# Kernel tuning notes

Measured on AMD Instinct MI355X. Metric: run time of the kernel, lower is better.

## Reference

```python
import jax, jax.numpy as jnp
import numpy as np

IMG, P, C = 512, 16, 1
D, DEPTH, H, DH, MLP = 768, 12, 8, 64, 2048
GRID = IMG // P          # 32
NP = GRID * GRID         # 1024 patches
N = NP + 1               # +cls token
EPS = 1e-5


def _ln(x, s, b):
    m = jnp.mean(x, -1, keepdims=True)
    v = jnp.mean((x - m) ** 2, -1, keepdims=True)
    return (x - m) * jax.lax.rsqrt(v + EPS) * s + b


def setup_inputs() -> dict:
    key = jax.random.key(0)
    ks = jax.random.split(key, 12)
    s = 0.02
    f32 = jnp.float32
    return {
        "x": jax.random.normal(ks[0], (4, C, IMG, IMG), f32),
        "conv_w": jax.random.normal(ks[1], (D, C, P, P), f32) * s,   # [out,in,kh,kw] like torch
        "conv_b": jnp.zeros((D,), f32),
        "cls_token": jax.random.normal(ks[2], (1, 1, D), f32),
        "pos_emb": jax.random.normal(ks[3], (1, N, D), f32),
        "qkv_w": jax.random.normal(ks[4], (DEPTH, D, 3 * H * DH), f32) * s,  # [in,out] layout
        "merge_w": jax.random.normal(ks[5], (DEPTH, H * DH, D), f32) * s,
        "merge_b": jnp.zeros((DEPTH, D), f32),
        "ln1_s": jnp.ones((DEPTH, D), f32),
        "ln1_b": jnp.zeros((DEPTH, D), f32),
        "ln2_s": jnp.ones((DEPTH, D), f32),
        "ln2_b": jnp.zeros((DEPTH, D), f32),
        "ffn_w1": jax.random.normal(ks[6], (DEPTH, D, MLP), f32) * s,
        "ffn_b1": jnp.zeros((DEPTH, MLP), f32),
        "ffn_w2": jax.random.normal(ks[7], (DEPTH, MLP, D), f32) * s,
        "ffn_b2": jnp.zeros((DEPTH, D), f32),
        "lnf_s": jnp.ones((D,), f32),
        "lnf_b": jnp.zeros((D,), f32),
    }


def reference(x, conv_w, conv_b, cls_token, pos_emb, qkv_w, merge_w, merge_b,
              ln1_s, ln1_b, ln2_s, ln2_b, ffn_w1, ffn_b1, ffn_w2, ffn_b2,
              lnf_s, lnf_b):
    B = x.shape[0]
    # Patch embed: stride-P conv == non-overlapping patch extraction + matmul
    xr = x.reshape(B, C, GRID, P, GRID, P)
    tok = jnp.einsum('bchpwq,dcpq->bhwd', xr, conv_w).reshape(B, NP, D) + conv_b
    t = jnp.concatenate([jnp.broadcast_to(cls_token, (B, 1, D)), tok], axis=1)
    t = t + pos_emb  # dropout is identity in eval
    scale = DH ** -0.5
    for i in range(DEPTH):
        # MSA with pre-LN
        h = _ln(t, ln1_s[i], ln1_b[i])
        qkv = (h @ qkv_w[i]).reshape(B, N, H, 3, DH)   # [B,N,H,3,DH]
        q = jnp.transpose(qkv[..., 0, :], (0, 2, 1, 3))  # [B,H,N,DH]
        k = jnp.transpose(qkv[..., 1, :], (0, 2, 1, 3))
        v = jnp.transpose(qkv[..., 2, :], (0, 2, 1, 3))
        att = jax.nn.softmax(jnp.einsum('bhnd,bhmd->bhnm', q, k) * scale, axis=-1)
        o = jnp.einsum('bhnm,bhmd->bhnd', att, v)
        o = jnp.transpose(o, (0, 2, 1, 3)).reshape(B, N, H * DH)
        t = t + (o @ merge_w[i] + merge_b[i])
        # FFN with pre-LN, exact (erf) GELU like torch nn.GELU
        h2 = _ln(t, ln2_s[i], ln2_b[i])
        f = jax.nn.gelu(h2 @ ffn_w1[i] + ffn_b1[i], approximate=False)
        t = t + (f @ ffn_w2[i] + ffn_b2[i])
    return _ln(t, lnf_s, lnf_b)
```

## Files before the change

### kernel.cpp

```cpp
#include <hip/hip_runtime.h>

#define DEV __device__ __forceinline__

typedef short s4v __attribute__((ext_vector_type(4)));
typedef short s8v __attribute__((ext_vector_type(8)));
typedef float f4v __attribute__((ext_vector_type(4)));
typedef unsigned int u32x2 __attribute__((ext_vector_type(2)));

DEV short f2bf(float f) {
  unsigned u = __float_as_uint(f);
  u += 0x7FFFu + ((u >> 16) & 1u);
  return (short)(u >> 16);
}
DEV short f2bf_fast(float f) {
  return (short)((__float_as_uint(f) + 0x8000u) >> 16);
}
DEV float bf2f(short s) { return __uint_as_float(((unsigned)(unsigned short)s) << 16); }

DEV void gld_lds16(const short* g, short* l) {
  __builtin_amdgcn_global_load_lds(
      (const __attribute__((address_space(1))) void*)g,
      (__attribute__((address_space(3))) void*)l, 16, 0, 0);
}

DEV u32x2 trr(unsigned lds_byte) {
  u32x2 r;
  asm volatile("ds_read_b64_tr_b16 %0, %1" : "=&v"(r) : "v"(lds_byte));
  return r;
}

DEV int xcd_swz(int id, int nwg) {
  int q8 = nwg >> 3, r8 = nwg & 7, xcd = id & 7, off = id >> 3;
  return (xcd < r8) ? (xcd * (q8 + 1) + off) : (r8 * (q8 + 1) + (xcd - r8) * q8 + off);
}

template<int BN>
__global__ __launch_bounds__(256) void gemm_t(
    const short* __restrict__ A, const short* __restrict__ B, void* __restrict__ Cv,
    const float* __restrict__ bias,
    int M, int N, int K, int lda, int ldb, int ldc, int flags)
{
  constexpr int BPASS = BN / 32;
  constexpr int MI = (BN == 128) ? 4 : 2;
  __shared__ __align__(16) short As[2][64 * 64];
  __shared__ __align__(16) short Bs[2][BN * 64];
  int nwg = gridDim.x * gridDim.y;
  int idl = blockIdx.y * gridDim.x + blockIdx.x;
  int swz = xcd_swz(idl, nwg);
  int bx = swz % gridDim.x, by = swz / gridDim.x;
  int m0 = by * 64, n0 = bx * BN;
  int tid = threadIdx.x, lane = tid & 63, w = tid >> 6;
  int lr = lane & 15, kg = lane >> 4;
  int wrb = (BN == 128) ? 0 : (w >> 1) * 32;
  int wcb = (BN == 128) ? w * 32 : (w & 1) * 32;
  f4v acc[MI][2] = {};
  int NT = K >> 6;

#define STAGE(bufi, k0)                                                   \
  {                                                                       \
    _Pragma("unroll")                                                     \
    for (int p = 0; p < 2; ++p) {                                         \
      int ch = p * 256 + w * 64 + lane;                                   \
      int row = ch >> 3, c = (ch & 7) ^ (row & 7);                        \
      gld_lds16(A + (long)(m0 + row) * lda + (k0) + c * 8,                \
                &As[bufi][(p * 256 + w * 64) * 8]);                       \
    }                                                                     \
    _Pragma("unroll")                                                     \
    for (int p = 0; p < BPASS; ++p) {                                     \
      int ch = p * 256 + w * 64 + lane;                                   \
      int row = ch >> 3, c = (ch & 7) ^ (row & 7);                        \
      gld_lds16(B + (long)(n0 + row) * ldb + (k0) + c * 8,                \
                &Bs[bufi][(p * 256 + w * 64) * 8]);                       \
    }                                                                     \
  }

  STAGE(0, 0)
  for (int t = 0; t < NT; ++t) {
    int buf = t & 1;
    if (t + 1 < NT) {
      STAGE(buf ^ 1, (t + 1) * 64)
      if constexpr (BN == 128)
        asm volatile("s_waitcnt vmcnt(6)" ::: "memory");
      else
        asm volatile("s_waitcnt vmcnt(4)" ::: "memory");
    } else {
      asm volatile("s_waitcnt vmcnt(0)" ::: "memory");
    }
    __builtin_amdgcn_s_barrier();
    #pragma unroll
    for (int ks = 0; ks < 2; ++ks) {
      s8v av[MI], bv[2];
      #pragma unroll
      for (int mi = 0; mi < MI; ++mi) {
        int row = wrb + mi * 16 + lr;
        int sl = (ks * 4 + kg) ^ (row & 7);
        av[mi] = *(const s8v*)&As[buf][row * 64 + sl * 8];
      }
      #pragma unroll
      for (int ni = 0; ni < 2; ++ni) {
        int row = wcb + ni * 16 + lr;
        int sl = (ks * 4 + kg) ^ (row & 7);
        bv[ni] = *(const s8v*)&Bs[buf][row * 64 + sl * 8];
      }
      #pragma unroll
      for (int mi = 0; mi < MI; ++mi)
        #pragma unroll
        for (int ni = 0; ni < 2; ++ni)
          acc[mi][ni] = __builtin_amdgcn_mfma_f32_16x16x32_bf16(av[mi], bv[ni], acc[mi][ni], 0, 0, 0);
    }
    asm volatile("s_waitcnt lgkmcnt(0)" ::: "memory");
    __builtin_amdgcn_s_barrier();
  }
#undef STAGE

  float* Cf = (float*)Cv;
  short* Cb = (short*)Cv;
  #pragma unroll
  for (int mi = 0; mi < MI; ++mi)
    #pragma unroll
    for (int ni = 0; ni < 2; ++ni) {
      int col = n0 + wcb + ni * 16 + lr;
      float bvv = (flags & 1) ? bias[col] : 0.f;
      #pragma unroll
      for (int j = 0; j < 4; ++j) {
        int row = m0 + wrb + mi * 16 + kg * 4 + j;
        if (row >= M) continue;
        float v = acc[mi][ni][j] + bvv;
        if (flags & 2) v = 0.5f * v * (1.f + erff(v * 0.70710678118f));
        long ci = (long)row * ldc + col;
        if (flags & 8) Cb[ci] = f2bf(v);
        else { if (flags & 4) v += Cf[ci]; Cf[ci] = v; }
      }
    }
}

__global__ __launch_bounds__(512) void flash_k(
    const short* __restrict__ qkv, short* __restrict__ O)
{
  int swz = xcd_swz(blockIdx.x, 544);
  int z = swz / 17, qt = swz - z * 17;
  int zb = z >> 3, zh = z & 7;
  const short* base = qkv + (long)zb * 1025 * 1536 + zh * 192;
  const short* Qg = base;
  const short* Kg = base + 64;
  const short* Vg = base + 128;
  int q0 = qt * 64;
  int tid = threadIdx.x, lane = tid & 63, w = tid >> 6;
  int g = w >> 2, wl = w & 3;
  int lr = lane & 15, kg = lane >> 4;
  int kt0 = g * 8;

  __shared__ __align__(16) short Ks[2][2][64 * 64];
  __shared__ __align__(16) short Vs[2][2][64 * 64];

  s8v aq[2];
  {
    long qrow = q0 + wl * 16 + lr;
    aq[0] = *(const s8v*)(Qg + qrow * 1536 + kg * 8);
    aq[1] = *(const s8v*)(Qg + qrow * 1536 + 32 + kg * 8);
  }

  unsigned vsbase = (unsigned)(unsigned long long)
      (__attribute__((address_space(3))) void*)&Vs[0][0][0];
  unsigned vtr = (unsigned)(lr * 8 + kg * 1024);

#define STAGE_K(bufi, kv0)                                                 \
  {                                                                        \
    int s0 = wl * 128;                                                     \
    _Pragma("unroll")                                                      \
    for (int i = 0; i < 2; ++i) {                                          \
      int s = s0 + i * 64 + lane;                                          \
      int row = s >> 3, c = (s & 7) ^ (row & 7);                           \
      gld_lds16(Kg + (long)((kv0) + row) * 1536 + c * 8,                   \
                &Ks[g][bufi][(s0 + i * 64) * 8]);                          \
    }                                                                      \
  }
#define STAGE_V(bufi, kv0)                                                 \
  {                                                                        \
    int s0 = wl * 128;                                                     \
    _Pragma("unroll")                                                      \
    for (int i = 0; i < 2; ++i) {                                          \
      int ch = s0 + i * 64 + lane;                                         \
      int st = ch >> 3, r = (ch & 7) >> 1, hh = ch & 1;                    \
      int key = (kv0) + (st >> 2) * 4 + r;                                 \
      int d = (st & 3) * 16 + hh * 8;                                      \
      gld_lds16(Vg + (long)key * 1536 + d,                                 \
                &Vs[g][bufi][(s0 + i * 64) * 8]);                          \
    }                                                                      \
  }

  f4v acc[4] = {};
  float m_run = -3.0e38f, l_run = 0.f;
  const float C2 = 0.18033688011112042f;
  const float THR = 44.36f;

  STAGE_K(0, kt0 * 64)
  STAGE_V(0, kt0 * 64)
  asm volatile("s_waitcnt vmcnt(0)" ::: "memory");
  __builtin_amdgcn_s_barrier();

  for (int kt = kt0; kt < kt0 + 8; ++kt) {
    int cur = (kt - kt0) & 1;
    if (kt + 1 < kt0 + 8) {
      STAGE_K(cur ^ 1, (kt + 1) * 64)
      STAGE_V(cur ^ 1, (kt + 1) * 64)
    }

    f4v sa[4] = {};
    __builtin_amdgcn_s_setprio(1);
    #pragma unroll
    for (int ni = 0; ni < 4; ++ni) {
      int row = ni * 16 + lr;
      #pragma unroll
      for (int ks = 0; ks < 2; ++ks) {
        int c = (ks * 4 + kg) ^ (row & 7);
        s8v kf = *(const s8v*)&Ks[g][cur][row * 64 + c * 8];
        sa[ni] = __builtin_amdgcn_mfma_f32_16x16x32_bf16(kf, aq[ks], sa[ni], 0, 0, 0);
      }
    }
    __builtin_amdgcn_s_setprio(0);

    float tm = -3.0e38f;
    #pragma unroll
    for (int ni = 0; ni < 4; ++ni)
      #pragma unroll
      for (int jj = 0; jj < 4; ++jj) tm = fmaxf(tm, sa[ni][jj]);
    tm = fmaxf(tm, __shfl_xor(tm, 16));
    tm = fmaxf(tm, __shfl_xor(tm, 32));
    bool need = !__all(tm <= m_run + THR);
    float scale = 1.f;
    if (need) {
      float m_new = fmaxf(m_run, tm);
      scale = exp2f((m_run - m_new) * C2);
      m_run = m_new;
    }
    float mC = m_run * C2;
    float pv[4][4];
    float ts = 0.f;
    #pragma unroll
    for (int ni = 0; ni < 4; ++ni)
      #pragma unroll
      for (int jj = 0; jj < 4; ++jj) {
        float p = exp2f(fmaf(sa[ni][jj], C2, -mC));
        pv[ni][jj] = p;
        ts += p;
      }
    ts += __shfl_xor(ts, 16);
    ts += __shfl_xor(ts, 32);
    l_run = l_run * scale + ts;
    if (need) {
      float scq[4];
      #pragma unroll
      for (int jj = 0; jj < 4; ++jj)
        scq[jj] = __shfl(scale, kg * 4 + jj + 16 * kg);
      #pragma unroll
      for (int ni = 0; ni < 4; ++ni)
        #pragma unroll
        for (int jj = 0; jj < 4; ++jj) acc[ni][jj] *= scq[jj];
    }

    unsigned pr[4][2];
    #pragma unroll
    for (int ni = 0; ni < 4; ++ni)
      #pragma unroll
      for (int hh = 0; hh < 2; ++hh) {
        unsigned lo = (unsigned)(unsigned short)f2bf_fast(pv[ni][2 * hh]);
        unsigned hi = (unsigned)(unsigned short)f2bf_fast(pv[ni][2 * hh + 1]);
        pr[ni][hh] = lo | (hi << 16);
      }
    union PU { s8v v; unsigned u[4]; };
    PU apu[2];
    #pragma unroll
    for (int ks = 0; ks < 2; ++ks)
      #pragma unroll
      for (int t = 0; t < 4; ++t) {
        unsigned src = (kg & 2) ? pr[2 * ks + 1][t & 1] : pr[2 * ks][t & 1];
        apu[ks].u[t] = __shfl(src, lr + 16 * (2 * (kg & 1) + (t >> 1)));
      }

    u32x2 tr[4][2][2];
    unsigned vb = vsbase + (unsigned)(g * 2 + cur) * 8192u + vtr;
    #pragma unroll
    for (int ni = 0; ni < 4; ++ni)
      #pragma unroll
      for (int ks = 0; ks < 2; ++ks) {
        tr[ni][ks][0] = trr(vb + ni * 128 + ks * 4096);
        tr[ni][ks][1] = trr(vb + ni * 128 + ks * 4096 + 512);
      }
    asm volatile("s_waitcnt lgkmcnt(0)" ::: "memory");
    __builtin_amdgcn_sched_barrier(0);

    __builtin_amdgcn_s_setprio(1);
    #pragma unroll
    for (int ni = 0; ni < 4; ++ni) {
      #pragma unroll
      for (int ks = 0; ks < 2; ++ks) {
        union { s8v v; u32x2 u2[2]; } bb;
        bb.u2[0] = tr[ni][ks][0];
        bb.u2[1] = tr[ni][ks][1];
        acc[ni] = __builtin_amdgcn_mfma_f32_16x16x32_bf16(apu[ks].v, bb.v, acc[ni], 0, 0, 0);
      }
    }
    __builtin_amdgcn_s_setprio(0);
    asm volatile("s_waitcnt lgkmcnt(0)" ::: "memory");
    asm volatile("s_waitcnt vmcnt(0)" ::: "memory");
    __builtin_amdgcn_s_barrier();
  }
#undef STAGE_K
#undef STAGE_V

  if (g) {
    s8v k0 = *(const s8v*)(Kg + 1024L * 1536 + kg * 8);
    s8v k1 = *(const s8v*)(Kg + 1024L * 1536 + 32 + kg * 8);
    float s = 0.f;
    #pragma unroll
    for (int j = 0; j < 8; ++j)
      s += bf2f(aq[0][j]) * bf2f(k0[j]) + bf2f(aq[1][j]) * bf2f(k1[j]);
    s += __shfl_xor(s, 16);
    s += __shfl_xor(s, 32);
    float m_new = fmaxf(m_run, s);
    float sc = exp2f((m_run - m_new) * C2);
    float p = exp2f((s - m_new) * C2);
    m_run = m_new;
    l_run = l_run * sc + p;
    float vrow[4];
    #pragma unroll
    for (int ni = 0; ni < 4; ++ni)
      vrow[ni] = bf2f(Vg[1024L * 1536 + ni * 16 + lr]);
    float scq[4], pq[4];
    #pragma unroll
    for (int jj = 0; jj < 4; ++jj) {
      scq[jj] = __shfl(sc, kg * 4 + jj + 16 * kg);
      pq[jj]  = __shfl(p,  kg * 4 + jj + 16 * kg);
    }
    #pragma unroll
    for (int ni = 0; ni < 4; ++ni)
      #pragma unroll
      for (int jj = 0; jj < 4; ++jj)
        acc[ni][jj] = acc[ni][jj] * scq[jj] + pq[jj] * vrow[ni];
  }

  float* AccL = (float*)&Ks[0][0][0];
  float* MLs  = (float*)&Vs[0][0][0];
  if (kg == 0) {
    MLs[(g * 64 + wl * 16 + lr) * 2]     = m_run;
    MLs[(g * 64 + wl * 16 + lr) * 2 + 1] = l_run;
  }
  if (g == 0) {
    #pragma unroll
    for (int ni = 0; ni < 4; ++ni)
      #pragma unroll
      for (int jj = 0; jj < 4; ++jj)
        AccL[(wl * 16 + kg * 4 + jj) * 64 + ni * 16 + lr] = acc[ni][jj];
  }
  asm volatile("s_waitcnt lgkmcnt(0)" ::: "memory");
  __builtin_amdgcn_s_barrier();
  if (g == 1) {
    float m0 = MLs[(wl * 16 + lr) * 2], l0 = MLs[(wl * 16 + lr) * 2 + 1];
    float M = fmaxf(m0, m_run);
    float w0 = exp2f((m0 - M) * C2), w1 = exp2f((m_run - M) * C2);
    float inv = 1.f / (l0 * w0 + l_run * w1);
    float c0 = w0 * inv, c1 = w1 * inv;
    float c0q[4], c1q[4];
    #pragma unroll
    for (int jj = 0; jj < 4; ++jj) {
      c0q[jj] = __shfl(c0, kg * 4 + jj + 16 * kg);
      c1q[jj] = __shfl(c1, kg * 4 + jj + 16 * kg);
    }
    #pragma unroll
    for (int ni = 0; ni < 4; ++ni)
      #pragma unroll
      for (int jj = 0; jj < 4; ++jj) {
        int row = q0 + wl * 16 + kg * 4 + jj;
        if (row < 1025) {
          float a0 = AccL[(wl * 16 + kg * 4 + jj) * 64 + ni * 16 + lr];
          O[((long)(zb * 1025 + row)) * 512 + zh * 64 + ni * 16 + lr] =
              f2bf(a0 * c0q[jj] + acc[ni][jj] * c1q[jj]);
        }
      }
  }
}

DEV void tconv_body(const float* w, short* wt, int K, int N, int bx, int by, int tid)
{
  __shared__ float tile[32][33];
  int n0 = bx * 32, k0 = by * 32;
  int tx = tid & 31, ty = tid >> 5;
  #pragma unroll
  for (int j = 0; j < 4; ++j)
    tile[ty + j * 8][tx] = w[(long)(k0 + ty + j * 8) * N + n0 + tx];
  __syncthreads();
  #pragma unroll
  for (int j = 0; j < 4; ++j)
    wt[(long)(n0 + ty + j * 8) * K + k0 + tx] = f2bf(tile[tx][ty + j * 8]);
}

__global__ __launch_bounds__(256) void tconv4_k(
    const float* __restrict__ sq, const float* __restrict__ sm,
    const float* __restrict__ sf1, const float* __restrict__ sf2,
    short* __restrict__ dq, short* __restrict__ dm,
    short* __restrict__ df1, short* __restrict__ df2)
{
  int id = blockIdx.x, tid = threadIdx.x;
  if (id < 1152)       tconv_body(sq,  dq,  768, 1536, id % 48,          id / 48,          tid);
  else if (id < 1536)  tconv_body(sm,  dm,  512, 768,  (id - 1152) % 24, (id - 1152) / 24, tid);
  else if (id < 3072)  tconv_body(sf1, df1, 768, 2048, (id - 1536) % 64, (id - 1536) / 64, tid);
  else                 tconv_body(sf2, df2, 2048, 768, (id - 3072) % 24, (id - 3072) / 24, tid);
}

__global__ __launch_bounds__(256) void cvt_k(const float* __restrict__ in,
    short* __restrict__ out, int n)
{
  int i = blockIdx.x * 256 + threadIdx.x;
  if (i < n) out[i] = f2bf(in[i]);
}

DEV void st4(float* p, f4v v) { *(f4v*)p = v; }
DEV void st4(short* p, f4v v) {
  s4v o = { f2bf(v[0]), f2bf(v[1]), f2bf(v[2]), f2bf(v[3]) };
  *(s4v*)p = o;
}

template<typename OT>
__global__ __launch_bounds__(256) void ln_k(const float* __restrict__ x,
    const float* __restrict__ g, const float* __restrict__ b,
    OT* __restrict__ y, int rows)
{
  int row = blockIdx.x * 4 + (threadIdx.x >> 6);
  if (row >= rows) return;
  int lane = threadIdx.x & 63;
  const float* xr = x + (long)row * 768;
  f4v v[3];
  #pragma unroll
  for (int i = 0; i < 3; ++i) v[i] = *(const f4v*)(xr + i * 256 + lane * 4);
  float s = 0.f, s2 = 0.f;
  #pragma unroll
  for (int i = 0; i < 3; ++i)
    #pragma unroll
    for (int j = 0; j < 4; ++j) { s += v[i][j]; s2 += v[i][j] * v[i][j]; }
  #pragma unroll
  for (int o = 1; o < 64; o <<= 1) { s += __shfl_xor(s, o); s2 += __shfl_xor(s2, o); }
  float mean = s * (1.f / 768.f);
  float var = s2 * (1.f / 768.f) - mean * mean;
  float r = rsqrtf(var + 1e-5f);
  OT* yr = y + (long)row * 768;
  #pragma unroll
  for (int i = 0; i < 3; ++i) {
    f4v gg = *(const f4v*)(g + i * 256 + lane * 4);
    f4v bb = *(const f4v*)(b + i * 256 + lane * 4);
    f4v o;
    #pragma unroll
    for (int j = 0; j < 4; ++j) o[j] = (v[i][j] - mean) * r * gg[j] + bb[j];
    st4(yr + i * 256 + lane * 4, o);
  }
}

__global__ __launch_bounds__(256) void im2col_k(const float* __restrict__ x,
    short* __restrict__ A)
{
  int i = blockIdx.x * 256 + threadIdx.x;
  int k = i & 255, row = i >> 8;
  int px = k & 15, py = k >> 4;
  int gx = row & 31, gy = (row >> 5) & 31, b = row >> 10;
  A[i] = f2bf(x[((long)(b * 512) + gy * 16 + py) * 512 + gx * 16 + px]);
}

__global__ __launch_bounds__(256) void assemble_k(const short* __restrict__ tok,
    const float* __restrict__ cls, const float* __restrict__ pos, float* __restrict__ t)
{
  int i = blockIdx.x * 256 + threadIdx.x;
  int d = i % 768; int rn = i / 768; int n = rn % 1025; int b = rn / 1025;
  float v = (n == 0) ? cls[d] : bf2f(tok[((long)(b * 1024 + n - 1)) * 768 + d]);
  t[i] = v + pos[n * 768 + d];
}

extern "C" void kernel_launch(void* const* d_in, const int* in_sizes, int n_in,
                              void* d_out, int out_size, void* d_ws, size_t ws_size,
                              hipStream_t stream)
{
  const float* x       = (const float*)d_in[0];
  const float* conv_w  = (const float*)d_in[1];
  const float* conv_b  = (const float*)d_in[2];
  const float* cls     = (const float*)d_in[3];
  const float* pos     = (const float*)d_in[4];
  const float* qkv_w   = (const float*)d_in[5];
  const float* merge_w = (const float*)d_in[6];
  const float* merge_b = (const float*)d_in[7];
  const float* ln1_s   = (const float*)d_in[8];
  const float* ln1_b   = (const float*)d_in[9];
  const float* ln2_s   = (const float*)d_in[10];
  const float* ln2_b   = (const float*)d_in[11];
  const float* ffn_w1  = (const float*)d_in[12];
  const float* ffn_b1  = (const float*)d_in[13];
  const float* ffn_w2  = (const float*)d_in[14];
  const float* ffn_b2  = (const float*)d_in[15];
  const float* lnf_s   = (const float*)d_in[16];
  const float* lnf_b   = (const float*)d_in[17];

  char* wsp = (char*)d_ws;
  size_t o = 0;
  auto take = [&](size_t bytes) { char* r = wsp + o; o = (o + bytes + 255) & ~(size_t)255; return r; };
  short* wq   = (short*)take(1536ul * 768 * 2);
  short* wm   = (short*)take(768ul * 512 * 2);
  short* wf1  = (short*)take(2048ul * 768 * 2);
  short* wf2  = (short*)take(768ul * 2048 * 2);
  short* wcv  = (short*)take(768ul * 256 * 2);
  float* t    = (float*)take(4100ul * 768 * 4);
  char*  hO   = take(4352ul * 768 * 2);
  short* qkv  = (short*)take(4ul * 1025 * 1536 * 2);
  char*  fV   = take(4352ul * 2048 * 2);
  take(2ul << 20);

  short* h   = (short*)hO;
  short* O   = (short*)hO;
  short* f   = (short*)fV;
  short* imc = (short*)fV;
  short* tok = (short*)(fV + 4096ul * 256 * 2);

  dim3 blk(256), blk512(512);

  cvt_k<<<768, blk, 0, stream>>>(conv_w, wcv, 768 * 256);
  im2col_k<<<4096, blk, 0, stream>>>(x, imc);
  gemm_t<64><<<dim3(12, 64), blk, 0, stream>>>(imc, wcv, tok, conv_b,
      4096, 768, 256, 256, 256, 768, 1 | 8);
  assemble_k<<<12300, blk, 0, stream>>>(tok, cls, pos, t);

  for (int i = 0; i < 12; ++i) {
    tconv4_k<<<4608, blk, 0, stream>>>(
        qkv_w + (long)i * 768 * 1536, merge_w + (long)i * 512 * 768,
        ffn_w1 + (long)i * 768 * 2048, ffn_w2 + (long)i * 2048 * 768,
        wq, wm, wf1, wf2);

    ln_k<short><<<1025, blk, 0, stream>>>(t, ln1_s + i * 768, ln1_b + i * 768, h, 4100);
    gemm_t<64><<<dim3(24, 65), blk, 0, stream>>>(h, wq, qkv, nullptr,
        4100, 1536, 768, 768, 768, 1536, 8);
    flash_k<<<544, blk512, 0, stream>>>(qkv, O);
    gemm_t<64><<<dim3(12, 65), blk, 0, stream>>>(O, wm, t, merge_b + i * 768,
        4100, 768, 512, 512, 512, 768, 1 | 4);
    ln_k<short><<<1025, blk, 0, stream>>>(t, ln2_s + i * 768, ln2_b + i * 768, h, 4100);
    gemm_t<64><<<dim3(32, 65), blk, 0, stream>>>(h, wf1, f, ffn_b1 + i * 2048,
        4100, 2048, 768, 768, 768, 2048, 1 | 2 | 8);
    gemm_t<64><<<dim3(12, 65), blk, 0, stream>>>(f, wf2, t, ffn_b2 + i * 768,
        4100, 768, 2048, 2048, 2048, 768, 1 | 4);
  }
  ln_k<float><<<1025, blk, 0, stream>>>(t, lnf_s, lnf_b, (float*)d_out, 4100);
}
```

Before: 1.969 ms.

## Split-K the N=768 projection GEMMs and fold partial-sum reduction into LayerNorm

The merge and FFN2 GEMMs, which have only 12x65 tiles, now run with a 2-way K split into two fp32 partial buffers, giving twice as many workgroups to fill the GPU. The following LayerNorm kernel adds both partials into the residual, writes the updated residual back, and normalizes it. This replaces the read-modify-write residual epilogue. The cost is extra fp32 partial-buffer traffic, about 25MB of writes and reads per GEMM, and an extra residual store in the LN kernel.

```diff
diff --git a/kernel.cpp b/kernel.cpp
--- a/kernel.cpp
+++ b/kernel.cpp
@@ -38,7 +38,7 @@
 __global__ __launch_bounds__(256) void gemm_t(
     const short* __restrict__ A, const short* __restrict__ B, void* __restrict__ Cv,
     const float* __restrict__ bias,
-    int M, int N, int K, int lda, int ldb, int ldc, int flags)
+    int M, int N, int K, int lda, int ldb, int ldc, int flags, int ksplit, long zCoff)
 {
   constexpr int BPASS = BN / 32;
   constexpr int MI = (BN == 128) ? 4 : 2;
@@ -54,7 +54,9 @@
   int wrb = (BN == 128) ? 0 : (w >> 1) * 32;
   int wcb = (BN == 128) ? w * 32 : (w & 1) * 32;
   f4v acc[MI][2] = {};
-  int NT = K >> 6;
+  int KH = K / ksplit;
+  int kbase = blockIdx.z * KH;
+  int NT = KH >> 6;
 
 #define STAGE(bufi, k0)                                                   \
   {                                                                       \
@@ -74,11 +76,11 @@
     }                                                                     \
   }
 
-  STAGE(0, 0)
+  STAGE(0, kbase)
   for (int t = 0; t < NT; ++t) {
     int buf = t & 1;
     if (t + 1 < NT) {
-      STAGE(buf ^ 1, (t + 1) * 64)
+      STAGE(buf ^ 1, kbase + (t + 1) * 64)
       if constexpr (BN == 128)
         asm volatile("s_waitcnt vmcnt(6)" ::: "memory");
       else
@@ -113,14 +115,15 @@
   }
 #undef STAGE
 
-  float* Cf = (float*)Cv;
-  short* Cb = (short*)Cv;
+  float* Cf = (float*)Cv + blockIdx.z * zCoff;
+  short* Cb = (short*)Cv + blockIdx.z * zCoff;
+  bool dob = (flags & 1) && blockIdx.z == 0;
   #pragma unroll
   for (int mi = 0; mi < MI; ++mi)
     #pragma unroll
     for (int ni = 0; ni < 2; ++ni) {
       int col = n0 + wcb + ni * 16 + lr;
-      float bvv = (flags & 1) ? bias[col] : 0.f;
+      float bvv = dob ? bias[col] : 0.f;
       #pragma unroll
       for (int j = 0; j < 4; ++j) {
         int row = m0 + wrb + mi * 16 + kg * 4 + j;
@@ -423,16 +426,30 @@
 
 template<typename OT>
 __global__ __launch_bounds__(256) void ln_k(const float* __restrict__ x,
+    const float* __restrict__ P0, const float* __restrict__ P1,
     const float* __restrict__ g, const float* __restrict__ b,
-    OT* __restrict__ y, int rows)
+    OT* __restrict__ y, float* __restrict__ xout, int rows)
 {
   int row = blockIdx.x * 4 + (threadIdx.x >> 6);
   if (row >= rows) return;
   int lane = threadIdx.x & 63;
-  const float* xr = x + (long)row * 768;
+  long rb = (long)row * 768;
   f4v v[3];
   #pragma unroll
-  for (int i = 0; i < 3; ++i) v[i] = *(const f4v*)(xr + i * 256 + lane * 4);
+  for (int i = 0; i < 3; ++i) v[i] = *(const f4v*)(x + rb + i * 256 + lane * 4);
+  if (P0) {
+    #pragma unroll
+    for (int i = 0; i < 3; ++i) {
+      f4v p0 = *(const f4v*)(P0 + rb + i * 256 + lane * 4);
+      f4v p1 = *(const f4v*)(P1 + rb + i * 256 + lane * 4);
+      #pragma unroll
+      for (int j = 0; j < 4; ++j) v[i][j] += p0[j] + p1[j];
+    }
+    if (xout) {
+      #pragma unroll
+      for (int i = 0; i < 3; ++i) st4(xout + rb + i * 256 + lane * 4, v[i]);
+    }
+  }
   float s = 0.f, s2 = 0.f;
   #pragma unroll
   for (int i = 0; i < 3; ++i)
@@ -443,7 +460,7 @@
   float mean = s * (1.f / 768.f);
   float var = s2 * (1.f / 768.f) - mean * mean;
   float r = rsqrtf(var + 1e-5f);
-  OT* yr = y + (long)row * 768;
+  OT* yr = y + rb;
   #pragma unroll
   for (int i = 0; i < 3; ++i) {
     f4v gg = *(const f4v*)(g + i * 256 + lane * 4);
@@ -506,6 +523,7 @@
   short* wf2  = (short*)take(768ul * 2048 * 2);
   short* wcv  = (short*)take(768ul * 256 * 2);
   float* t    = (float*)take(4100ul * 768 * 4);
+  float* PA   = (float*)take(2ul * 4100 * 768 * 4);
   char*  hO   = take(4352ul * 768 * 2);
   short* qkv  = (short*)take(4ul * 1025 * 1536 * 2);
   char*  fV   = take(4352ul * 2048 * 2);
@@ -516,13 +534,14 @@
   short* f   = (short*)fV;
   short* imc = (short*)fV;
   short* tok = (short*)(fV + 4096ul * 256 * 2);
+  const long PZ = 4100L * 768;
 
   dim3 blk(256), blk512(512);
 
   cvt_k<<<768, blk, 0, stream>>>(conv_w, wcv, 768 * 256);
   im2col_k<<<4096, blk, 0, stream>>>(x, imc);
   gemm_t<64><<<dim3(12, 64), blk, 0, stream>>>(imc, wcv, tok, conv_b,
-      4096, 768, 256, 256, 256, 768, 1 | 8);
+      4096, 768, 256, 256, 256, 768, 1 | 8, 1, 0);
   assemble_k<<<12300, blk, 0, stream>>>(tok, cls, pos, t);
 
   for (int i = 0; i < 12; ++i) {
@@ -531,17 +550,20 @@
         ffn_w1 + (long)i * 768 * 2048, ffn_w2 + (long)i * 2048 * 768,
         wq, wm, wf1, wf2);
 
-    ln_k<short><<<1025, blk, 0, stream>>>(t, ln1_s + i * 768, ln1_b + i * 768, h, 4100);
+    ln_k<short><<<1025, blk, 0, stream>>>(t, i ? PA : nullptr, PA + PZ,
+        ln1_s + i * 768, ln1_b + i * 768, h, t, 4100);
     gemm_t<64><<<dim3(24, 65), blk, 0, stream>>>(h, wq, qkv, nullptr,
-        4100, 1536, 768, 768, 768, 1536, 8);
+        4100, 1536, 768, 768, 768, 1536, 8, 1, 0);
     flash_k<<<544, blk512, 0, stream>>>(qkv, O);
-    gemm_t<64><<<dim3(12, 65), blk, 0, stream>>>(O, wm, t, merge_b + i * 768,
-        4100, 768, 512, 512, 512, 768, 1 | 4);
-    ln_k<short><<<1025, blk, 0, stream>>>(t, ln2_s + i * 768, ln2_b + i * 768, h, 4100);
+    gemm_t<64><<<dim3(12, 65, 2), blk, 0, stream>>>(O, wm, PA, merge_b + i * 768,
+        4100, 768, 512, 512, 512, 768, 1, 2, PZ);
+    ln_k<short><<<1025, blk, 0, stream>>>(t, PA, PA + PZ,
+        ln2_s + i * 768, ln2_b + i * 768, h, t, 4100);
     gemm_t<64><<<dim3(32, 65), blk, 0, stream>>>(h, wf1, f, ffn_b1 + i * 2048,
-        4100, 2048, 768, 768, 768, 2048, 1 | 2 | 8);
-    gemm_t<64><<<dim3(12, 65), blk, 0, stream>>>(f, wf2, t, ffn_b2 + i * 768,
-        4100, 768, 2048, 2048, 2048, 768, 1 | 4);
-  }
-  ln_k<float><<<1025, blk, 0, stream>>>(t, lnf_s, lnf_b, (float*)d_out, 4100);
-}
+        4100, 2048, 768, 768, 768, 2048, 1 | 2 | 8, 1, 0);
+    gemm_t<64><<<dim3(12, 65, 2), blk, 0, stream>>>(f, wf2, PA, ffn_b2 + i * 768,
+        4100, 768, 2048, 2048, 2048, 768, 1, 2, PZ);
+  }
+  ln_k<float><<<1025, blk, 0, stream>>>(t, PA, PA + PZ,
+      lnf_s, lnf_b, (float*)d_out, nullptr, 4100);
+}
```

Result: slower. 2.088 ms (+6.0%).
